# Performance work log

Measured on AMD Instinct MI355X. Metric: run time of the kernel, lower is better.

Reference implementation:

```python
import jax, jax.numpy as jnp
import numpy as np

MARGIN = 0.5          # TripletLoss(margin=0.5)
N_FEAT = 100000       # gallery size N (rows of `features`)
D = 128               # embedding dim
N_BATCH = 256         # batch size n
N_CLASSES = 1000      # number of identities -> ~100 positives per class


def setup_inputs() -> dict:
    key = jax.random.key(0)
    k1, k2 = jax.random.split(key)
    inputs = jax.random.normal(k1, (N_BATCH, D), dtype=jnp.float32)
    features = jax.random.normal(k2, (N_FEAT, D), dtype=jnp.float32)
    # feature_labels encodes the t2i dict: label of every gallery row.
    feature_labels = (jnp.arange(N_FEAT, dtype=jnp.int32) % N_CLASSES).astype(jnp.int32)
    # idx[i] is the gallery row corresponding to batch sample i (distinct rows).
    idx = jnp.arange(N_BATCH, dtype=jnp.int32)
    # consistency: targets[i] must equal feature_labels[idx[i]]
    targets = feature_labels[idx]
    return {"inputs": inputs, "features": features, "targets": targets,
            "feature_labels": feature_labels, "idx": idx}


def reference(inputs, features, targets, feature_labels, idx):
    # sim_mat = inputs @ features.T  -> [n, N]
    sim = jnp.matmul(inputs, features.T)
    n_feat = features.shape[0]
    # pos: same identity, excluding the sample's own gallery row idx[i]
    same = feature_labels[None, :] == targets[:, None]          # [n, N]
    is_self = jnp.arange(n_feat, dtype=idx.dtype)[None, :] == idx[:, None]
    pos_mask = same & ~is_self
    neg_mask = ~same
    big = jnp.asarray(jnp.finfo(sim.dtype).max, sim.dtype)
    pos = jnp.min(jnp.where(pos_mask, sim, big), axis=1)        # hardest positive (min sim)
    neg = jnp.max(jnp.where(neg_mask, sim, -big), axis=1)       # hardest negative (max sim)
    loss = jax.nn.relu(neg - pos + MARGIN)                      # [n]
    return jnp.sum(loss) / targets.shape[0]
```

## Files before the change

kernel.cpp:

```cpp
#include <hip/hip_runtime.h>

#define NFEAT   100000
#define NBATCH  256
#define DIM     128
#define MARGIN_F 0.5f
#define GRID    625
#define RPB     160
#define NTILE   10
#define BBYTES  (RPB * DIM * 4)
#define FLT_BIG 3.402823466e+38f

typedef __bf16 bf8_t  __attribute__((ext_vector_type(8)));
typedef short  sh8_t  __attribute__((ext_vector_type(8)));
typedef float  f32x4  __attribute__((ext_vector_type(4)));

__device__ __forceinline__ bf8_t pack8(float4 v0, float4 v1) {
  bf8_t r;
  r[0] = (__bf16)v0.x; r[1] = (__bf16)v0.y; r[2] = (__bf16)v0.z; r[3] = (__bf16)v0.w;
  r[4] = (__bf16)v1.x; r[5] = (__bf16)v1.y; r[6] = (__bf16)v1.z; r[7] = (__bf16)v1.w;
  return r;
}

template <typename VA, typename VC>
__device__ __forceinline__ auto mfma_sel(VA a, VA b, VC c, int)
    -> decltype(__builtin_amdgcn_mfma_f32_16x16x32_bf16(a, b, c, 0, 0, 0)) {
  return __builtin_amdgcn_mfma_f32_16x16x32_bf16(a, b, c, 0, 0, 0);
}
template <typename VA, typename VC>
__device__ __forceinline__ VC mfma_sel(VA a, VA b, VC c, long) {
  return __builtin_amdgcn_mfma_f32_16x16x32_bf16(
      __builtin_bit_cast(sh8_t, a), __builtin_bit_cast(sh8_t, b), c, 0, 0, 0);
}
__device__ __forceinline__ f32x4 mfma_bf16(bf8_t a, bf8_t b, f32x4 c) {
  return mfma_sel(a, b, c, 0);
}

#if defined(__has_builtin)
#if __has_builtin(__builtin_amdgcn_global_load_lds)
#define HAVE_GLLDS 1
#endif
#endif

__device__ __forceinline__ void stage16(const char* g, char* l) {
#ifdef HAVE_GLLDS
  __builtin_amdgcn_global_load_lds(
      (const __attribute__((address_space(1))) unsigned int*)g,
      (__attribute__((address_space(3))) unsigned int*)l, 16, 0, 0);
#else
  *reinterpret_cast<float4*>(l) = *reinterpret_cast<const float4*>(g);
#endif
}

__global__ __launch_bounds__(512, 2) void triplet_partial(
    const float* __restrict__ inputs, const float* __restrict__ features,
    const int* __restrict__ targets, const int* __restrict__ flabels,
    const int* __restrict__ idx,
    float* __restrict__ ppos, float* __restrict__ pneg,
    float* __restrict__ out)
{
  __shared__ char sB[BBYTES];

  const int tid  = threadIdx.x;
  const int lane = tid & 63;
  const int wv   = tid >> 6;
  const int l15  = lane & 15;
  const int lg   = lane >> 4;
  const int m0   = wv * 32;
  const int blk  = blockIdx.x;
  const int rowbase = blk * RPB;

  if (blk == 0 && tid == 0) out[0] = 0.0f;

#pragma unroll
  for (int i = 0; i < NTILE; ++i) {
    const int p    = i * 8192 + tid * 16;
    const int prow = p >> 9;
    const int scol = (p & 511) ^ ((prow & 7) << 4);
    stage16((const char*)features + (size_t)(rowbase + prow) * 512 + scol,
            &sB[p]);
  }

  bf8_t afrag[2][4];
#pragma unroll
  for (int mt = 0; mt < 2; ++mt) {
    const float* ap = inputs + (m0 + mt * 16 + l15) * DIM;
    float4 v0[4], v1[4];
#pragma unroll
    for (int ks = 0; ks < 4; ++ks) {
      const int k = ks * 32 + lg * 8;
      v0[ks] = *reinterpret_cast<const float4*>(ap + k);
      v1[ks] = *reinterpret_cast<const float4*>(ap + k + 4);
    }
#pragma unroll
    for (int ks = 0; ks < 4; ++ks)
      afrag[mt][ks] = pack8(v0[ks], v1[ks]);
  }

  int lab[NTILE];
#pragma unroll
  for (int t = 0; t < NTILE; ++t)
    lab[t] = flabels[rowbase + t * 16 + l15];

  int meta[2][4];
#pragma unroll
  for (int mt = 0; mt < 2; ++mt)
#pragma unroll
    for (int rr = 0; rr < 4; ++rr) {
      const int row = m0 + mt * 16 + lg * 4 + rr;
      meta[mt][rr] = (idx[row] << 10) | targets[row];
    }

  float minpos[2][4], maxneg[2][4];
#pragma unroll
  for (int mt = 0; mt < 2; ++mt)
#pragma unroll
    for (int rr = 0; rr < 4; ++rr) { minpos[mt][rr] = FLT_BIG; maxneg[mt][rr] = -FLT_BIG; }

  __syncthreads();

  const int swz = (l15 & 7) << 4;
#pragma unroll
  for (int t = 0; t < NTILE; ++t) {
    const char* rbase = &sB[(t * 16 + l15) * 512];
    const int   j     = rowbase + t * 16 + l15;
    const int   labj  = lab[t];

    f32x4 acc0 = {0.f, 0.f, 0.f, 0.f};
    f32x4 acc1 = {0.f, 0.f, 0.f, 0.f};
#pragma unroll
    for (int ks = 0; ks < 4; ++ks) {
      const int o = ks * 128 + lg * 32;
      float4 v0 = *reinterpret_cast<const float4*>(rbase + ((o)      ^ swz));
      float4 v1 = *reinterpret_cast<const float4*>(rbase + ((o + 16) ^ swz));
      bf8_t bf = pack8(v0, v1);
      acc0 = mfma_bf16(afrag[0][ks], bf, acc0);
      acc1 = mfma_bf16(afrag[1][ks], bf, acc1);
    }

#pragma unroll
    for (int rr = 0; rr < 4; ++rr) {
      {
        const int   m    = meta[0][rr];
        const bool same  = (labj == (m & 1023));
        const bool self  = (j == (m >> 10));
        minpos[0][rr] = fminf(minpos[0][rr], (same && !self) ? acc0[rr] : FLT_BIG);
        maxneg[0][rr] = fmaxf(maxneg[0][rr], same ? -FLT_BIG : acc0[rr]);
      }
      {
        const int   m    = meta[1][rr];
        const bool same  = (labj == (m & 1023));
        const bool self  = (j == (m >> 10));
        minpos[1][rr] = fminf(minpos[1][rr], (same && !self) ? acc1[rr] : FLT_BIG);
        maxneg[1][rr] = fmaxf(maxneg[1][rr], same ? -FLT_BIG : acc1[rr]);
      }
    }
  }

#pragma unroll
  for (int mt = 0; mt < 2; ++mt)
#pragma unroll
    for (int rr = 0; rr < 4; ++rr) {
      float mp = minpos[mt][rr], mn = maxneg[mt][rr];
#pragma unroll
      for (int m = 1; m < 16; m <<= 1) {
        mp = fminf(mp, __shfl_xor(mp, m, 64));
        mn = fmaxf(mn, __shfl_xor(mn, m, 64));
      }
      if (l15 == 0) {
        const int row = m0 + mt * 16 + lg * 4 + rr;
        ppos[blk * NBATCH + row] = mp;
        pneg[blk * NBATCH + row] = mn;
      }
    }
}

__global__ __launch_bounds__(256) void triplet_reduce(
    const float* __restrict__ ppos, const float* __restrict__ pneg,
    float* __restrict__ out)
{
  const int r = blockIdx.x;
  const int t = threadIdx.x;
  float mp = FLT_BIG, mn = -FLT_BIG;
  for (int b = t; b < GRID; b += 256) {
    mp = fminf(mp, ppos[b * NBATCH + r]);
    mn = fmaxf(mn, pneg[b * NBATCH + r]);
  }
#pragma unroll
  for (int m = 1; m < 64; m <<= 1) {
    mp = fminf(mp, __shfl_xor(mp, m, 64));
    mn = fmaxf(mn, __shfl_xor(mn, m, 64));
  }
  __shared__ float smp[4], smn[4];
  if ((t & 63) == 0) { smp[t >> 6] = mp; smn[t >> 6] = mn; }
  __syncthreads();
  if (t == 0) {
    mp = fminf(fminf(smp[0], smp[1]), fminf(smp[2], smp[3]));
    mn = fmaxf(fmaxf(smn[0], smn[1]), fmaxf(smn[2], smn[3]));
    float loss = mn - mp + MARGIN_F;
    loss = loss > 0.f ? loss : 0.f;
    atomicAdd(out, loss * (1.0f / NBATCH));
  }
}

extern "C" void kernel_launch(void* const* d_in, const int* in_sizes, int n_in,
                              void* d_out, int out_size, void* d_ws, size_t ws_size,
                              hipStream_t stream) {
  const float* inputs   = (const float*)d_in[0];
  const float* features = (const float*)d_in[1];
  const int*   targets  = (const int*)d_in[2];
  const int*   flabels  = (const int*)d_in[3];
  const int*   idx      = (const int*)d_in[4];
  float* out  = (float*)d_out;
  float* ppos = (float*)d_ws;
  float* pneg = ppos + (size_t)GRID * NBATCH;

  triplet_partial<<<GRID, 512, 0, stream>>>(inputs, features, targets, flabels, idx, ppos, pneg, out);
  triplet_reduce<<<NBATCH, 256, 0, stream>>>(ppos, pneg, out);
}
```

Before: 47.07 us.

## Pre-convert gallery features to bf16 in a separate pass before the similarity kernel

Adds a conversion kernel that writes the features as bf16 into workspace, then runs the fused similarity/min-max kernel reading half-size rows into LDS. This removes in-loop fp32-to-bf16 packing and halves LDS footprint, but adds a full extra read and write pass over the gallery on every call. A fallback fp32 path with smaller blocks (80 rows, 1250 blocks) is used when the workspace is too small.

```diff
diff --git a/kernel.cpp b/kernel.cpp
--- a/kernel.cpp
+++ b/kernel.cpp
@@ -4,11 +4,16 @@
 #define NBATCH  256
 #define DIM     128
 #define MARGIN_F 0.5f
-#define GRID    625
-#define RPB     160
-#define NTILE   10
-#define BBYTES  (RPB * DIM * 4)
 #define FLT_BIG 3.402823466e+38f
+
+#define GRIDB   625
+#define RPBB    160
+#define NTILEB  10
+#define BBYTESB (RPBB * DIM * 2)
+
+#define GRIDF   1250
+#define RPBF    80
+#define NTILEF  5
 
 typedef __bf16 bf8_t  __attribute__((ext_vector_type(8)));
 typedef short  sh8_t  __attribute__((ext_vector_type(8)));
@@ -51,14 +56,29 @@
 #endif
 }
 
-__global__ __launch_bounds__(512, 2) void triplet_partial(
-    const float* __restrict__ inputs, const float* __restrict__ features,
+__global__ __launch_bounds__(256) void feat_to_bf16(
+    const float* __restrict__ src, __bf16* __restrict__ dst,
+    float* __restrict__ out)
+{
+  if (blockIdx.x == 0 && threadIdx.x == 0) out[0] = 0.0f;
+  const int gid    = blockIdx.x * 256 + threadIdx.x;
+  const int stride = gridDim.x * 256;
+  const int n8     = NFEAT * DIM / 8;
+  for (int i = gid; i < n8; i += stride) {
+    const float* p = src + (size_t)i * 8;
+    float4 v0 = *reinterpret_cast<const float4*>(p);
+    float4 v1 = *reinterpret_cast<const float4*>(p + 4);
+    *reinterpret_cast<bf8_t*>(dst + (size_t)i * 8) = pack8(v0, v1);
+  }
+}
+
+__global__ __launch_bounds__(512, 2) void triplet_partial_bf16(
+    const float* __restrict__ inputs, const __bf16* __restrict__ featb,
     const int* __restrict__ targets, const int* __restrict__ flabels,
     const int* __restrict__ idx,
-    float* __restrict__ ppos, float* __restrict__ pneg,
-    float* __restrict__ out)
+    float* __restrict__ ppos, float* __restrict__ pneg)
 {
-  __shared__ char sB[BBYTES];
+  __shared__ char sB[BBYTESB];
 
   const int tid  = threadIdx.x;
   const int lane = tid & 63;
@@ -67,16 +87,14 @@
   const int lg   = lane >> 4;
   const int m0   = wv * 32;
   const int blk  = blockIdx.x;
-  const int rowbase = blk * RPB;
-
-  if (blk == 0 && tid == 0) out[0] = 0.0f;
-
-#pragma unroll
-  for (int i = 0; i < NTILE; ++i) {
+  const int rowbase = blk * RPBB;
+
+#pragma unroll
+  for (int i = 0; i < NTILEB; ++i) {
     const int p    = i * 8192 + tid * 16;
-    const int prow = p >> 9;
-    const int scol = (p & 511) ^ ((prow & 7) << 4);
-    stage16((const char*)features + (size_t)(rowbase + prow) * 512 + scol,
+    const int prow = p >> 8;
+    const int scol = (p & 255) ^ ((prow & 7) << 4);
+    stage16((const char*)featb + (size_t)(rowbase + prow) * 256 + scol,
             &sB[p]);
   }
 
@@ -96,9 +114,9 @@
       afrag[mt][ks] = pack8(v0[ks], v1[ks]);
   }
 
-  int lab[NTILE];
-#pragma unroll
-  for (int t = 0; t < NTILE; ++t)
+  int lab[NTILEB];
+#pragma unroll
+  for (int t = 0; t < NTILEB; ++t)
     lab[t] = flabels[rowbase + t * 16 + l15];
 
   int meta[2][4];
@@ -120,7 +138,127 @@
 
   const int swz = (l15 & 7) << 4;
 #pragma unroll
-  for (int t = 0; t < NTILE; ++t) {
+  for (int t = 0; t < NTILEB; ++t) {
+    const char* rbase = &sB[(t * 16 + l15) * 256];
+    const int   j     = rowbase + t * 16 + l15;
+    const int   labj  = lab[t];
+
+    f32x4 acc0 = {0.f, 0.f, 0.f, 0.f};
+    f32x4 acc1 = {0.f, 0.f, 0.f, 0.f};
+#pragma unroll
+    for (int ks = 0; ks < 4; ++ks) {
+      const int o = (ks * 64 + lg * 16) ^ swz;
+      bf8_t bf = *reinterpret_cast<const bf8_t*>(rbase + o);
+      acc0 = mfma_bf16(afrag[0][ks], bf, acc0);
+      acc1 = mfma_bf16(afrag[1][ks], bf, acc1);
+    }
+
+#pragma unroll
+    for (int rr = 0; rr < 4; ++rr) {
+      {
+        const int   m    = meta[0][rr];
+        const bool same  = (labj == (m & 1023));
+        const bool self  = (j == (m >> 10));
+        minpos[0][rr] = fminf(minpos[0][rr], (same && !self) ? acc0[rr] : FLT_BIG);
+        maxneg[0][rr] = fmaxf(maxneg[0][rr], same ? -FLT_BIG : acc0[rr]);
+      }
+      {
+        const int   m    = meta[1][rr];
+        const bool same  = (labj == (m & 1023));
+        const bool self  = (j == (m >> 10));
+        minpos[1][rr] = fminf(minpos[1][rr], (same && !self) ? acc1[rr] : FLT_BIG);
+        maxneg[1][rr] = fmaxf(maxneg[1][rr], same ? -FLT_BIG : acc1[rr]);
+      }
+    }
+  }
+
+#pragma unroll
+  for (int mt = 0; mt < 2; ++mt)
+#pragma unroll
+    for (int rr = 0; rr < 4; ++rr) {
+      float mp = minpos[mt][rr], mn = maxneg[mt][rr];
+#pragma unroll
+      for (int m = 1; m < 16; m <<= 1) {
+        mp = fminf(mp, __shfl_xor(mp, m, 64));
+        mn = fmaxf(mn, __shfl_xor(mn, m, 64));
+      }
+      if (l15 == 0) {
+        const int row = m0 + mt * 16 + lg * 4 + rr;
+        ppos[blk * NBATCH + row] = mp;
+        pneg[blk * NBATCH + row] = mn;
+      }
+    }
+}
+
+__global__ __launch_bounds__(512, 2) void triplet_partial_f32(
+    const float* __restrict__ inputs, const float* __restrict__ features,
+    const int* __restrict__ targets, const int* __restrict__ flabels,
+    const int* __restrict__ idx,
+    float* __restrict__ ppos, float* __restrict__ pneg,
+    float* __restrict__ out)
+{
+  __shared__ char sB[RPBF * DIM * 4];
+
+  const int tid  = threadIdx.x;
+  const int lane = tid & 63;
+  const int wv   = tid >> 6;
+  const int l15  = lane & 15;
+  const int lg   = lane >> 4;
+  const int m0   = wv * 32;
+  const int blk  = blockIdx.x;
+  const int rowbase = blk * RPBF;
+
+  if (blk == 0 && tid == 0) out[0] = 0.0f;
+
+#pragma unroll
+  for (int i = 0; i < NTILEF; ++i) {
+    const int p    = i * 8192 + tid * 16;
+    const int prow = p >> 9;
+    const int scol = (p & 511) ^ ((prow & 7) << 4);
+    stage16((const char*)features + (size_t)(rowbase + prow) * 512 + scol, &sB[p]);
+  }
+
+  bf8_t afrag[2][4];
+#pragma unroll
+  for (int mt = 0; mt < 2; ++mt) {
+    const float* ap = inputs + (m0 + mt * 16 + l15) * DIM;
+    float4 v0[4], v1[4];
+#pragma unroll
+    for (int ks = 0; ks < 4; ++ks) {
+      const int k = ks * 32 + lg * 8;
+      v0[ks] = *reinterpret_cast<const float4*>(ap + k);
+      v1[ks] = *reinterpret_cast<const float4*>(ap + k + 4);
+    }
+#pragma unroll
+    for (int ks = 0; ks < 4; ++ks)
+      afrag[mt][ks] = pack8(v0[ks], v1[ks]);
+  }
+
+  int lab[NTILEF];
+#pragma unroll
+  for (int t = 0; t < NTILEF; ++t)
+    lab[t] = flabels[rowbase + t * 16 + l15];
+
+  int meta[2][4];
+#pragma unroll
+  for (int mt = 0; mt < 2; ++mt)
+#pragma unroll
+    for (int rr = 0; rr < 4; ++rr) {
+      const int row = m0 + mt * 16 + lg * 4 + rr;
+      meta[mt][rr] = (idx[row] << 10) | targets[row];
+    }
+
+  float minpos[2][4], maxneg[2][4];
+#pragma unroll
+  for (int mt = 0; mt < 2; ++mt)
+#pragma unroll
+    for (int rr = 0; rr < 4; ++rr) { minpos[mt][rr] = FLT_BIG; maxneg[mt][rr] = -FLT_BIG; }
+
+  __syncthreads();
+
+  const int swz = (l15 & 7) << 4;
+#pragma unroll
+  for (int t = 0; t < NTILEF; ++t) {
     const char* rbase = &sB[(t * 16 + l15) * 512];
     const int   j     = rowbase + t * 16 + l15;
     const int   labj  = lab[t];
@@ -136,20 +274,19 @@
       acc0 = mfma_bf16(afrag[0][ks], bf, acc0);
       acc1 = mfma_bf16(afrag[1][ks], bf, acc1);
     }
-
 #pragma unroll
     for (int rr = 0; rr < 4; ++rr) {
       {
-        const int   m    = meta[0][rr];
-        const bool same  = (labj == (m & 1023));
-        const bool self  = (j == (m >> 10));
+        const int  m = meta[0][rr];
+        const bool same = (labj == (m & 1023));
+        const bool self = (j == (m >> 10));
         minpos[0][rr] = fminf(minpos[0][rr], (same && !self) ? acc0[rr] : FLT_BIG);
         maxneg[0][rr] = fmaxf(maxneg[0][rr], same ? -FLT_BIG : acc0[rr]);
       }
       {
-        const int   m    = meta[1][rr];
-        const bool same  = (labj == (m & 1023));
-        const bool self  = (j == (m >> 10));
+        const int  m = meta[1][rr];
+        const bool same = (labj == (m & 1023));
+        const bool self = (j == (m >> 10));
         minpos[1][rr] = fminf(minpos[1][rr], (same && !self) ? acc1[rr] : FLT_BIG);
         maxneg[1][rr] = fmaxf(maxneg[1][rr], same ? -FLT_BIG : acc1[rr]);
       }
@@ -176,12 +313,12 @@
 
 __global__ __launch_bounds__(256) void triplet_reduce(
     const float* __restrict__ ppos, const float* __restrict__ pneg,
-    float* __restrict__ out)
+    float* __restrict__ out, int nblk)
 {
   const int r = blockIdx.x;
   const int t = threadIdx.x;
   float mp = FLT_BIG, mn = -FLT_BIG;
-  for (int b = t; b < GRID; b += 256) {
+  for (int b = t; b < nblk; b += 256) {
     mp = fminf(mp, ppos[b * NBATCH + r]);
     mn = fmaxf(mn, pneg[b * NBATCH + r]);
   }
@@ -210,10 +347,24 @@
   const int*   targets  = (const int*)d_in[2];
   const int*   flabels  = (const int*)d_in[3];
   const int*   idx      = (const int*)d_in[4];
-  float* out  = (float*)d_out;
-  float* ppos = (float*)d_ws;
-  float* pneg = ppos + (size_t)GRID * NBATCH;
-
-  triplet_partial<<<GRID, 512, 0, stream>>>(inputs, features, targets, flabels, idx, ppos, pneg, out);
-  triplet_reduce<<<NBATCH, 256, 0, stream>>>(ppos, pneg, out);
-}
+  float* out = (float*)d_out;
+
+  const size_t featb_bytes = (size_t)NFEAT * DIM * 2;
+  const size_t part_bytes  = (size_t)GRIDB * NBATCH * 4;
+
+  if (ws_size >= featb_bytes + 2 * part_bytes) {
+    __bf16* featb = (__bf16*)d_ws;
+    float*  ppos  = (float*)((char*)d_ws + featb_bytes);
+    float*  pneg  = ppos + (size_t)GRIDB * NBATCH;
+    feat_to_bf16<<<2048, 256, 0, stream>>>(features, featb, out);
+    triplet_partial_bf16<<<GRIDB, 512, 0, stream>>>(inputs, featb, targets,
+                                                    flabels, idx, ppos, pneg);
+    triplet_reduce<<<NBATCH, 256, 0, stream>>>(ppos, pneg, out, GRIDB);
+  } else {
+    float* ppos = (float*)d_ws;
+    float* pneg = ppos + (size_t)GRIDF * NBATCH;
+    triplet_partial_f32<<<GRIDF, 512, 0, stream>>>(inputs, features, targets,
+                                                   flabels, idx, ppos, pneg, out);
+    triplet_reduce<<<NBATCH, 256, 0, stream>>>(ppos, pneg, out, GRIDF);
+  }
+}
```

After: 53.60 us. +13.9%, slower.
